# Kernel optimization log

Hardware: AMD Instinct MI355X
Metric: run time of the kernel (lower is better)

## Reference

```python
import jax, jax.numpy as jnp
import numpy as np

Q_DIM = 512
K_DIM = 512
V_DIM = 512
H_DIM = 256
B, Q, K = 4, 512, 512


def setup_inputs() -> dict:
    key = jax.random.key(0)
    ks = jax.random.split(key, 7)
    q = jax.random.normal(ks[0], (B, Q, Q_DIM), dtype=jnp.float32)
    k = jax.random.normal(ks[1], (B, K, K_DIM), dtype=jnp.float32)
    v = jax.random.normal(ks[2], (B, K, V_DIM), dtype=jnp.float32)
    S = jax.random.randint(ks[3], (B,), 1, K + 1, dtype=jnp.int64)
    # learned params (nn.Linear stores weight of shape (out, in); y = x @ W.T)
    Wq = jax.random.normal(ks[4], (H_DIM, Q_DIM), dtype=jnp.float32) / np.sqrt(Q_DIM)
    Wk = jax.random.normal(ks[5], (H_DIM, K_DIM), dtype=jnp.float32) / np.sqrt(K_DIM)
    w = jax.random.normal(ks[6], (H_DIM,), dtype=jnp.float32) / np.sqrt(H_DIM)
    return {"q": q, "k": k, "v": v, "S": S, "Wq": Wq, "Wk": Wk, "w": w}


def reference(q, k, v, S, Wq, Wk, w):
    # Additive (Bahdanau) attention scores.
    pq = jnp.einsum('bqd,hd->bqh', q, Wq)            # (B, Q, H)
    pk = jnp.einsum('bkd,hd->bkh', k, Wk)            # (B, K, H)
    t = jnp.tanh(pq[:, :, None, :] + pk[:, None, :, :])  # (B, Q, K, H)
    scores = jnp.einsum('bqkh,h->bqk', t, w)         # (B, Q, K)
    # mask keys with index >= S[b] to -inf
    kv_idx = jnp.arange(scores.shape[-1])            # (K,)
    mask = kv_idx[None, None, :] >= S[:, None, None] # (B, 1, K) -> broadcast
    scores = jnp.where(mask, -jnp.inf, scores)
    return scores
```

## Files before the change

### kernel.cpp

```cpp
#include <hip/hip_runtime.h>
#include <hip/hip_bf16.h>
#include <math.h>

#define QDIM 512
#define HDIM 256
#define QQ 512
#define KKE 512

#define TWO_LOG2E 2.8853900817779268f
#define MASK_VAL -1.0e30f

typedef __attribute__((ext_vector_type(8))) short bf16x8;
typedef __attribute__((ext_vector_type(4))) float f32x4;

__device__ __forceinline__ unsigned int pk2(float x, float y) {
  __hip_bfloat162 h = __float22bfloat162_rn(make_float2(x, y));
  unsigned int u;
  __builtin_memcpy(&u, &h, 4);
  return u;
}

__global__ __launch_bounds__(512) void proj_kernel(
    const float* __restrict__ qin, const float* __restrict__ kin,
    const float* __restrict__ Wq, const float* __restrict__ Wk,
    const float* __restrict__ wvec,
    float* __restrict__ EqT, unsigned short* __restrict__ EkT,
    float* __restrict__ wsum_out) {
  __shared__ __align__(16) unsigned short As[32 * 72];
  __shared__ __align__(16) unsigned short Bs[64 * 72];

  const int tid = threadIdx.x;
  const int lane = tid & 63;
  const int wv = __builtin_amdgcn_readfirstlane(tid >> 6);
  const int quad = lane >> 4;
  const int l16 = lane & 15;

  const int m0 = blockIdx.x * 32;
  const int h0 = blockIdx.y * 64;
  const bool isk = (blockIdx.z != 0);
  const float* A = isk ? kin : qin;
  const float* W = isk ? Wk : Wq;

  const int srow = tid >> 4;
  const int sg = (tid & 15) * 4;

  const float* arow_g = &A[(size_t)(m0 + srow) * QDIM + sg];
  const float* brow0_g = &W[(size_t)(h0 + srow) * QDIM + sg];
  const float* brow1_g = &W[(size_t)(h0 + srow + 32) * QDIM + sg];
  unsigned short* adst = &As[srow * 72 + sg];
  unsigned short* bdst0 = &Bs[srow * 72 + sg];
  unsigned short* bdst1 = &Bs[(srow + 32) * 72 + sg];

  const unsigned short* afrag = &As[((wv & 1) * 16 + l16) * 72 + quad * 8];
  const unsigned short* bfrag = &Bs[((wv >> 1) * 16 + l16) * 72 + quad * 8];

  f32x4 acc = (f32x4){0.f, 0.f, 0.f, 0.f};

  float4 pa = *(const float4*)arow_g;
  float4 pb0 = *(const float4*)brow0_g;
  float4 pb1 = *(const float4*)brow1_g;

  for (int kc = 0; kc < QDIM; kc += 64) {
    __syncthreads();
    *(uint2*)adst = make_uint2(pk2(pa.x, pa.y), pk2(pa.z, pa.w));
    *(uint2*)bdst0 = make_uint2(pk2(pb0.x, pb0.y), pk2(pb0.z, pb0.w));
    *(uint2*)bdst1 = make_uint2(pk2(pb1.x, pb1.y), pk2(pb1.z, pb1.w));
    if (kc + 64 < QDIM) {
      pa = *(const float4*)(arow_g + kc + 64);
      pb0 = *(const float4*)(brow0_g + kc + 64);
      pb1 = *(const float4*)(brow1_g + kc + 64);
    }
    __syncthreads();
    bf16x8 a0 = *(const bf16x8*)afrag;
    bf16x8 a1 = *(const bf16x8*)(afrag + 32);
    bf16x8 b0 = *(const bf16x8*)bfrag;
    bf16x8 b1 = *(const bf16x8*)(bfrag + 32);
    acc = __builtin_amdgcn_mfma_f32_16x16x32_bf16(a0, b0, acc, 0, 0, 0);
    acc = __builtin_amdgcn_mfma_f32_16x16x32_bf16(a1, b1, acc, 0, 0, 0);
  }

  const int b = m0 >> 9;
  const int hrow = h0 + (wv >> 1) * 16 + l16;
  const int mcol = (m0 & 511) + (wv & 1) * 16 + quad * 4;
  float e0 = __builtin_amdgcn_exp2f(acc[0] * TWO_LOG2E);
  float e1 = __builtin_amdgcn_exp2f(acc[1] * TWO_LOG2E);
  float e2 = __builtin_amdgcn_exp2f(acc[2] * TWO_LOG2E);
  float e3 = __builtin_amdgcn_exp2f(acc[3] * TWO_LOG2E);
  if (!isk) {
    *(float4*)(EqT + ((size_t)b * HDIM + hrow) * 512 + mcol) =
        make_float4(e0, e1, e2, e3);
    if (m0 == 0 && h0 == 0 && tid < 64) {
      float s = wvec[tid] + wvec[tid + 64] + wvec[tid + 128] + wvec[tid + 192];
#pragma unroll
      for (int off = 32; off; off >>= 1) s += __shfl_down(s, off);
      if (tid == 0) wsum_out[0] = s;
    }
  } else {
    *(uint2*)(EkT + ((size_t)b * HDIM + hrow) * 512 + mcol) =
        make_uint2(pk2(e0, e1), pk2(e2, e3));
  }
}

__global__ __launch_bounds__(256) void score_kernel(
    const float* __restrict__ EqT, const unsigned short* __restrict__ EkT,
    const float* __restrict__ wvec, const float* __restrict__ wsump,
    const int* __restrict__ Sraw, float* __restrict__ out) {
  const int b = blockIdx.z;
  const int q0 = blockIdx.y * 16;
  const int i = blockIdx.x;
  const int S = (Sraw[1] == 0) ? Sraw[2 * b] : Sraw[b];
  const int tid = threadIdx.x;
  const int wv = __builtin_amdgcn_readfirstlane(tid >> 6);
  const int L = tid & 63;
  const int q = L >> 2;
  const int k8 = (L & 3) * 8;

  __shared__ float wl[HDIM];
  __shared__ float Eqs[256][16];
  __shared__ unsigned short Eks[256][32];
  __shared__ float Cmb[3][64][8];
  wl[tid] = wvec[tid];

  const float wsum = wsump[0];
  const float* EqB = EqT + (size_t)b * (HDIM * QQ) + q0;
  const unsigned short* EkB0 = EkT + (size_t)b * (HDIM * KKE);

#pragma unroll
  for (int t = 0; t < 2; ++t) {
    const int kt = t ? (15 - i) : i;
    const int k0 = kt * 32;
    float* orow = out + ((size_t)(b * QQ + q0 + q) * KKE + k0 + k8);

    if (k0 >= S) {
      if (wv == 0) {
        float4 m4 = make_float4(MASK_VAL, MASK_VAL, MASK_VAL, MASK_VAL);
        *(float4*)&orow[0] = m4;
        *(float4*)&orow[4] = m4;
      }
      continue;
    }

    __syncthreads();
    {
      const unsigned short* EkB = EkB0 + k0;
      const int hr = tid >> 2;
      const int cq = (tid & 3) * 4;
      const int ce = (tid & 3) * 8;
#pragma unroll
      for (int p = 0; p < 4; p++) {
        *(float4*)&Eqs[hr + p * 64][cq] =
            *(const float4*)&EqB[(size_t)(hr + p * 64) * QQ + cq];
        *(uint4*)&Eks[hr + p * 64][ce] =
            *(const uint4*)&EkB[(size_t)(hr + p * 64) * KKE + ce];
      }
    }
    __syncthreads();

    float a0 = 0.f, a1 = 0.f, a2 = 0.f, a3 = 0.f;
    float a4 = 0.f, a5 = 0.f, a6 = 0.f, a7 = 0.f;
    const int hbase = wv * 64;
#pragma unroll 4
    for (int hh = 0; hh < 64; hh++) {
      const int h = hbase + hh;
      float wh = wl[h];
      float eq = Eqs[h][q];
      uint4 u = *(const uint4*)&Eks[h][k8];
      float e0 = __uint_as_float(u.x << 16);
      float e1 = __uint_as_float(u.x & 0xffff0000u);
      float e2 = __uint_as_float(u.y << 16);
      float e3 = __uint_as_float(u.y & 0xffff0000u);
      float e4 = __uint_as_float(u.z << 16);
      float e5 = __uint_as_float(u.z & 0xffff0000u);
      float e6 = __uint_as_float(u.w << 16);
      float e7 = __uint_as_float(u.w & 0xffff0000u);
      a0 = fmaf(wh, __builtin_amdgcn_rcpf(fmaf(eq, e0, 1.f)), a0);
      a1 = fmaf(wh, __builtin_amdgcn_rcpf(fmaf(eq, e1, 1.f)), a1);
      a2 = fmaf(wh, __builtin_amdgcn_rcpf(fmaf(eq, e2, 1.f)), a2);
      a3 = fmaf(wh, __builtin_amdgcn_rcpf(fmaf(eq, e3, 1.f)), a3);
      a4 = fmaf(wh, __builtin_amdgcn_rcpf(fmaf(eq, e4, 1.f)), a4);
      a5 = fmaf(wh, __builtin_amdgcn_rcpf(fmaf(eq, e5, 1.f)), a5);
      a6 = fmaf(wh, __builtin_amdgcn_rcpf(fmaf(eq, e6, 1.f)), a6);
      a7 = fmaf(wh, __builtin_amdgcn_rcpf(fmaf(eq, e7, 1.f)), a7);
    }

    if (wv > 0) {
      Cmb[wv - 1][L][0] = a0; Cmb[wv - 1][L][1] = a1;
      Cmb[wv - 1][L][2] = a2; Cmb[wv - 1][L][3] = a3;
      Cmb[wv - 1][L][4] = a4; Cmb[wv - 1][L][5] = a5;
      Cmb[wv - 1][L][6] = a6; Cmb[wv - 1][L][7] = a7;
    }
    __syncthreads();
    if (wv == 0) {
#pragma unroll
      for (int c = 0; c < 3; c++) {
        a0 += Cmb[c][L][0]; a1 += Cmb[c][L][1];
        a2 += Cmb[c][L][2]; a3 += Cmb[c][L][3];
        a4 += Cmb[c][L][4]; a5 += Cmb[c][L][5];
        a6 += Cmb[c][L][6]; a7 += Cmb[c][L][7];
      }
      const int kb = k0 + k8;
      float4 r0, r1;
      r0.x = (kb + 0 < S) ? (wsum - 2.f * a0) : MASK_VAL;
      r0.y = (kb + 1 < S) ? (wsum - 2.f * a1) : MASK_VAL;
      r0.z = (kb + 2 < S) ? (wsum - 2.f * a2) : MASK_VAL;
      r0.w = (kb + 3 < S) ? (wsum - 2.f * a3) : MASK_VAL;
      r1.x = (kb + 4 < S) ? (wsum - 2.f * a4) : MASK_VAL;
      r1.y = (kb + 5 < S) ? (wsum - 2.f * a5) : MASK_VAL;
      r1.z = (kb + 6 < S) ? (wsum - 2.f * a6) : MASK_VAL;
      r1.w = (kb + 7 < S) ? (wsum - 2.f * a7) : MASK_VAL;
      *(float4*)&orow[0] = r0;
      *(float4*)&orow[4] = r1;
    }
  }
}

extern "C" void kernel_launch(void* const* d_in, const int* in_sizes, int n_in,
                              void* d_out, int out_size, void* d_ws, size_t ws_size,
                              hipStream_t stream) {
  const float* q  = (const float*)d_in[0];
  const float* k  = (const float*)d_in[1];
  const int*   S  = (const int*)d_in[3];
  const float* Wq = (const float*)d_in[4];
  const float* Wk = (const float*)d_in[5];
  const float* w  = (const float*)d_in[6];
  float* out = (float*)d_out;

  float* wsf = (float*)d_ws;
  float* EqT = wsf;
  unsigned short* EkT = (unsigned short*)(wsf + 524288);
  float* wsum = wsf + 524288 + 262144;

  proj_kernel<<<dim3(64, 4, 2), 512, 0, stream>>>(q, k, Wq, Wk, w, EqT, EkT, wsum);
  score_kernel<<<dim3(8, 32, 4), 256, 0, stream>>>(EqT, EkT, w, wsum, S, out);
}
```

Baseline: 97.44 us.

## Store Eq as bf16, double-buffer proj LDS, prefetch both score tiles up front

The projection kernel now writes exp(2*Eq) as bf16 instead of fp32 and double-buffers its LDS tiles, which removes one barrier per k-step. The score kernel issues the global loads for both key tiles before any compute, so the second tile's fetch overlaps the first tile's work. It exits early when both tiles are fully masked. The cross-wave reduction is spread over all four waves, with 16 lanes of each wave finishing their own rows, instead of being funnelled through wave 0. Storing Eq in bf16 halves its memory traffic but adds rounding error, and the held prefetch registers raise register pressure.

```diff
diff --git a/kernel.cpp b/kernel.cpp
--- a/kernel.cpp
+++ b/kernel.cpp
@@ -24,10 +24,10 @@
     const float* __restrict__ qin, const float* __restrict__ kin,
     const float* __restrict__ Wq, const float* __restrict__ Wk,
     const float* __restrict__ wvec,
-    float* __restrict__ EqT, unsigned short* __restrict__ EkT,
+    unsigned short* __restrict__ EqT, unsigned short* __restrict__ EkT,
     float* __restrict__ wsum_out) {
-  __shared__ __align__(16) unsigned short As[32 * 72];
-  __shared__ __align__(16) unsigned short Bs[64 * 72];
+  __shared__ __align__(16) unsigned short As[2][32 * 72];
+  __shared__ __align__(16) unsigned short Bs[2][64 * 72];
 
   const int tid = threadIdx.x;
   const int lane = tid & 63;
@@ -47,12 +47,10 @@
   const float* arow_g = &A[(size_t)(m0 + srow) * QDIM + sg];
   const float* brow0_g = &W[(size_t)(h0 + srow) * QDIM + sg];
   const float* brow1_g = &W[(size_t)(h0 + srow + 32) * QDIM + sg];
-  unsigned short* adst = &As[srow * 72 + sg];
-  unsigned short* bdst0 = &Bs[srow * 72 + sg];
-  unsigned short* bdst1 = &Bs[(srow + 32) * 72 + sg];
-
-  const unsigned short* afrag = &As[((wv & 1) * 16 + l16) * 72 + quad * 8];
-  const unsigned short* bfrag = &Bs[((wv >> 1) * 16 + l16) * 72 + quad * 8];
+  const int aoff = srow * 72 + sg;
+  const int boff1 = (srow + 32) * 72 + sg;
+  const int afo = ((wv & 1) * 16 + l16) * 72 + quad * 8;
+  const int bfo = ((wv >> 1) * 16 + l16) * 72 + quad * 8;
 
   f32x4 acc = (f32x4){0.f, 0.f, 0.f, 0.f};
 
@@ -60,21 +58,21 @@
   float4 pb0 = *(const float4*)brow0_g;
   float4 pb1 = *(const float4*)brow1_g;
 
-  for (int kc = 0; kc < QDIM; kc += 64) {
-    __syncthreads();
-    *(uint2*)adst = make_uint2(pk2(pa.x, pa.y), pk2(pa.z, pa.w));
-    *(uint2*)bdst0 = make_uint2(pk2(pb0.x, pb0.y), pk2(pb0.z, pb0.w));
-    *(uint2*)bdst1 = make_uint2(pk2(pb1.x, pb1.y), pk2(pb1.z, pb1.w));
+  int ib = 0;
+  for (int kc = 0; kc < QDIM; kc += 64, ib ^= 1) {
+    *(uint2*)&As[ib][aoff] = make_uint2(pk2(pa.x, pa.y), pk2(pa.z, pa.w));
+    *(uint2*)&Bs[ib][aoff] = make_uint2(pk2(pb0.x, pb0.y), pk2(pb0.z, pb0.w));
+    *(uint2*)&Bs[ib][boff1] = make_uint2(pk2(pb1.x, pb1.y), pk2(pb1.z, pb1.w));
     if (kc + 64 < QDIM) {
       pa = *(const float4*)(arow_g + kc + 64);
       pb0 = *(const float4*)(brow0_g + kc + 64);
       pb1 = *(const float4*)(brow1_g + kc + 64);
     }
     __syncthreads();
-    bf16x8 a0 = *(const bf16x8*)afrag;
-    bf16x8 a1 = *(const bf16x8*)(afrag + 32);
-    bf16x8 b0 = *(const bf16x8*)bfrag;
-    bf16x8 b1 = *(const bf16x8*)(bfrag + 32);
+    bf16x8 a0 = *(const bf16x8*)&As[ib][afo];
+    bf16x8 a1 = *(const bf16x8*)&As[ib][afo + 32];
+    bf16x8 b0 = *(const bf16x8*)&Bs[ib][bfo];
+    bf16x8 b1 = *(const bf16x8*)&Bs[ib][bfo + 32];
     acc = __builtin_amdgcn_mfma_f32_16x16x32_bf16(a0, b0, acc, 0, 0, 0);
     acc = __builtin_amdgcn_mfma_f32_16x16x32_bf16(a1, b1, acc, 0, 0, 0);
   }
@@ -86,23 +84,19 @@
   float e1 = __builtin_amdgcn_exp2f(acc[1] * TWO_LOG2E);
   float e2 = __builtin_amdgcn_exp2f(acc[2] * TWO_LOG2E);
   float e3 = __builtin_amdgcn_exp2f(acc[3] * TWO_LOG2E);
-  if (!isk) {
-    *(float4*)(EqT + ((size_t)b * HDIM + hrow) * 512 + mcol) =
-        make_float4(e0, e1, e2, e3);
-    if (m0 == 0 && h0 == 0 && tid < 64) {
-      float s = wvec[tid] + wvec[tid + 64] + wvec[tid + 128] + wvec[tid + 192];
-#pragma unroll
-      for (int off = 32; off; off >>= 1) s += __shfl_down(s, off);
-      if (tid == 0) wsum_out[0] = s;
-    }
-  } else {
-    *(uint2*)(EkT + ((size_t)b * HDIM + hrow) * 512 + mcol) =
-        make_uint2(pk2(e0, e1), pk2(e2, e3));
+  unsigned short* ET = isk ? EkT : EqT;
+  *(uint2*)(ET + ((size_t)b * HDIM + hrow) * 512 + mcol) =
+      make_uint2(pk2(e0, e1), pk2(e2, e3));
+  if (!isk && m0 == 0 && h0 == 0 && tid < 64) {
+    float s = wvec[tid] + wvec[tid + 64] + wvec[tid + 128] + wvec[tid + 192];
+#pragma unroll
+    for (int off = 32; off; off >>= 1) s += __shfl_down(s, off);
+    if (tid == 0) wsum_out[0] = s;
   }
 }
 
 __global__ __launch_bounds__(256) void score_kernel(
-    const float* __restrict__ EqT, const unsigned short* __restrict__ EkT,
+    const unsigned short* __restrict__ EqT, const unsigned short* __restrict__ EkT,
     const float* __restrict__ wvec, const float* __restrict__ wsump,
     const int* __restrict__ Sraw, float* __restrict__ out) {
   const int b = blockIdx.z;
@@ -116,54 +110,62 @@
   const int k8 = (L & 3) * 8;
 
   __shared__ float wl[HDIM];
-  __shared__ float Eqs[256][16];
+  __shared__ unsigned short Eqs[256][16];
   __shared__ unsigned short Eks[256][32];
-  __shared__ float Cmb[3][64][8];
-  wl[tid] = wvec[tid];
+  __shared__ float Cmb[4][64][8];
+
+  const int kt0 = i;
+  const int kt1 = 15 - i;
+  const bool live0 = (kt0 * 32) < S;
+  const bool live1 = (kt1 * 32) < S;
+
+  const int mq = 4 * wv + (L >> 2);
+  const int mkg = (L & 3) * 8;
+  float* mrow0 = out + ((size_t)(b * QQ + q0 + mq) * KKE) + kt0 * 32 + mkg;
+  float* mrow1 = out + ((size_t)(b * QQ + q0 + mq) * KKE) + kt1 * 32 + mkg;
+  const float4 m4 = make_float4(MASK_VAL, MASK_VAL, MASK_VAL, MASK_VAL);
+
+  if (!live0) {
+    if (L < 16) {
+      *(float4*)&mrow0[0] = m4; *(float4*)&mrow0[4] = m4;
+      *(float4*)&mrow1[0] = m4; *(float4*)&mrow1[4] = m4;
+    }
+    return;
+  }
 
   const float wsum = wsump[0];
-  const float* EqB = EqT + (size_t)b * (HDIM * QQ) + q0;
-  const unsigned short* EkB0 = EkT + (size_t)b * (HDIM * KKE);
-
-#pragma unroll
-  for (int t = 0; t < 2; ++t) {
-    const int kt = t ? (15 - i) : i;
-    const int k0 = kt * 32;
-    float* orow = out + ((size_t)(b * QQ + q0 + q) * KKE + k0 + k8);
-
-    if (k0 >= S) {
-      if (wv == 0) {
-        float4 m4 = make_float4(MASK_VAL, MASK_VAL, MASK_VAL, MASK_VAL);
-        *(float4*)&orow[0] = m4;
-        *(float4*)&orow[4] = m4;
-      }
-      continue;
-    }
-
-    __syncthreads();
-    {
-      const unsigned short* EkB = EkB0 + k0;
-      const int hr = tid >> 2;
-      const int cq = (tid & 3) * 4;
-      const int ce = (tid & 3) * 8;
-#pragma unroll
-      for (int p = 0; p < 4; p++) {
-        *(float4*)&Eqs[hr + p * 64][cq] =
-            *(const float4*)&EqB[(size_t)(hr + p * 64) * QQ + cq];
-        *(uint4*)&Eks[hr + p * 64][ce] =
-            *(const uint4*)&EkB[(size_t)(hr + p * 64) * KKE + ce];
-      }
-    }
-    __syncthreads();
-
+  const float wreg = wvec[tid];
+  const unsigned short* EqB = EqT + (size_t)b * (HDIM * QQ) + q0;
+  const unsigned short* EkB = EkT + (size_t)b * (HDIM * KKE);
+  const int hr = tid >> 2;
+  const int ce = (tid & 3) * 8;
+
+  uint4 qa = *(const uint4*)(EqB + (size_t)tid * QQ);
+  uint4 qb = *(const uint4*)(EqB + (size_t)tid * QQ + 8);
+  uint4 k0r[4], k1r[4];
+#pragma unroll
+  for (int p = 0; p < 4; p++)
+    k0r[p] = *(const uint4*)(EkB + (size_t)(hr + p * 64) * KKE + kt0 * 32 + ce);
+#pragma unroll
+  for (int p = 0; p < 4; p++)
+    k1r[p] = *(const uint4*)(EkB + (size_t)(hr + p * 64) * KKE + kt1 * 32 + ce);
+
+  wl[tid] = wreg;
+  *(uint4*)&Eqs[tid][0] = qa;
+  *(uint4*)&Eqs[tid][8] = qb;
+#pragma unroll
+  for (int p = 0; p < 4; p++) *(uint4*)&Eks[hr + p * 64][ce] = k0r[p];
+  __syncthreads();
+
+  const int hbase = wv * 64;
+  auto tile_pass = [&]() {
     float a0 = 0.f, a1 = 0.f, a2 = 0.f, a3 = 0.f;
     float a4 = 0.f, a5 = 0.f, a6 = 0.f, a7 = 0.f;
-    const int hbase = wv * 64;
 #pragma unroll 4
     for (int hh = 0; hh < 64; hh++) {
       const int h = hbase + hh;
       float wh = wl[h];
-      float eq = Eqs[h][q];
+      float eq = __uint_as_float((unsigned int)Eqs[h][q] << 16);
       uint4 u = *(const uint4*)&Eks[h][k8];
       float e0 = __uint_as_float(u.x << 16);
       float e1 = __uint_as_float(u.x & 0xffff0000u);
@@ -182,36 +184,54 @@
       a6 = fmaf(wh, __builtin_amdgcn_rcpf(fmaf(eq, e6, 1.f)), a6);
       a7 = fmaf(wh, __builtin_amdgcn_rcpf(fmaf(eq, e7, 1.f)), a7);
     }
-
-    if (wv > 0) {
-      Cmb[wv - 1][L][0] = a0; Cmb[wv - 1][L][1] = a1;
-      Cmb[wv - 1][L][2] = a2; Cmb[wv - 1][L][3] = a3;
-      Cmb[wv - 1][L][4] = a4; Cmb[wv - 1][L][5] = a5;
-      Cmb[wv - 1][L][6] = a6; Cmb[wv - 1][L][7] = a7;
-    }
-    __syncthreads();
-    if (wv == 0) {
-#pragma unroll
-      for (int c = 0; c < 3; c++) {
-        a0 += Cmb[c][L][0]; a1 += Cmb[c][L][1];
-        a2 += Cmb[c][L][2]; a3 += Cmb[c][L][3];
-        a4 += Cmb[c][L][4]; a5 += Cmb[c][L][5];
-        a6 += Cmb[c][L][6]; a7 += Cmb[c][L][7];
+    *(float4*)&Cmb[wv][L][0] = make_float4(a0, a1, a2, a3);
+    *(float4*)&Cmb[wv][L][4] = make_float4(a4, a5, a6, a7);
+  };
+
+  auto sum_store = [&](float* mrow, int kbase) {
+    if (L < 16) {
+      const int Ls = (mq << 2) | (L & 3);
+      float s0 = 0.f, s1 = 0.f, s2 = 0.f, s3 = 0.f;
+      float s4 = 0.f, s5 = 0.f, s6 = 0.f, s7 = 0.f;
+#pragma unroll
+      for (int w = 0; w < 4; w++) {
+        float4 c0 = *(const float4*)&Cmb[w][Ls][0];
+        float4 c1 = *(const float4*)&Cmb[w][Ls][4];
+        s0 += c0.x; s1 += c0.y; s2 += c0.z; s3 += c0.w;
+        s4 += c1.x; s5 += c1.y; s6 += c1.z; s7 += c1.w;
       }
-      const int kb = k0 + k8;
+      const int kb = kbase + mkg;
       float4 r0, r1;
-      r0.x = (kb + 0 < S) ? (wsum - 2.f * a0) : MASK_VAL;
-      r0.y = (kb + 1 < S) ? (wsum - 2.f * a1) : MASK_VAL;
-      r0.z = (kb + 2 < S) ? (wsum - 2.f * a2) : MASK_VAL;
-      r0.w = (kb + 3 < S) ? (wsum - 2.f * a3) : MASK_VAL;
-      r1.x = (kb + 4 < S) ? (wsum - 2.f * a4) : MASK_VAL;
-      r1.y = (kb + 5 < S) ? (wsum - 2.f * a5) : MASK_VAL;
-      r1.z = (kb + 6 < S) ? (wsum - 2.f * a6) : MASK_VAL;
-      r1.w = (kb + 7 < S) ? (wsum - 2.f * a7) : MASK_VAL;
-      *(float4*)&orow[0] = r0;
-      *(float4*)&orow[4] = r1;
-    }
-  }
+      r0.x = (kb + 0 < S) ? (wsum - 2.f * s0) : MASK_VAL;
+      r0.y = (kb + 1 < S) ? (wsum - 2.f * s1) : MASK_VAL;
+      r0.z = (kb + 2 < S) ? (wsum - 2.f * s2) : MASK_VAL;
+      r0.w = (kb + 3 < S) ? (wsum - 2.f * s3) : MASK_VAL;
+      r1.x = (kb + 4 < S) ? (wsum - 2.f * s4) : MASK_VAL;
+      r1.y = (kb + 5 < S) ? (wsum - 2.f * s5) : MASK_VAL;
+      r1.z = (kb + 6 < S) ? (wsum - 2.f * s6) : MASK_VAL;
+      r1.w = (kb + 7 < S) ? (wsum - 2.f * s7) : MASK_VAL;
+      *(float4*)&mrow[0] = r0;
+      *(float4*)&mrow[4] = r1;
+    }
+  };
+
+  tile_pass();
+  __syncthreads();
+  if (live1) {
+#pragma unroll
+    for (int p = 0; p < 4; p++) *(uint4*)&Eks[hr + p * 64][ce] = k1r[p];
+  }
+  sum_store(mrow0, kt0 * 32);
+
+  if (!live1) {
+    if (L < 16) { *(float4*)&mrow1[0] = m4; *(float4*)&mrow1[4] = m4; }
+    return;
+  }
+
+  __syncthreads();
+  tile_pass();
+  __syncthreads();
+  sum_store(mrow1, kt1 * 32);
 }
 
 extern "C" void kernel_launch(void* const* d_in, const int* in_sizes, int n_in,
@@ -225,10 +245,9 @@
   const float* w  = (const float*)d_in[6];
   float* out = (float*)d_out;
 
-  float* wsf = (float*)d_ws;
-  float* EqT = wsf;
-  unsigned short* EkT = (unsigned short*)(wsf + 524288);
-  float* wsum = wsf + 524288 + 262144;
+  unsigned short* EqT = (unsigned short*)d_ws;
+  unsigned short* EkT = EqT + 524288;
+  float* wsum = (float*)(EkT + 524288);
 
   proj_kernel<<<dim3(64, 4, 2), 512, 0, stream>>>(q, k, Wq, Wk, w, EqT, EkT, wsum);
   score_kernel<<<dim3(8, 32, 4), 256, 0, stream>>>(EqT, EkT, w, wsum, S, out);
```

Result: slower. 99.86 us (+2.5%).

## Process four k-tiles per block with prefetched Ek and reused Eq tile

Applied to the files above, without the earlier changes.

Each score block now handles four k-tiles instead of two, loading the Eq tile once and reusing it across all of them. The next Ek tile is prefetched into registers while the current tile computes, then written to shared memory. Ek is widened to fp32 in shared memory so the inner loop no longer unpacks bf16. The final reduction is split across all four waves instead of done by wave 0 alone. This halves the grid to 512 blocks and doubles shared memory for Ek, which lowers parallelism and may reduce occupancy.

```diff
diff --git a/kernel.cpp b/kernel.cpp
--- a/kernel.cpp
+++ b/kernel.cpp
@@ -117,99 +117,134 @@
 
   __shared__ float wl[HDIM];
   __shared__ float Eqs[256][16];
-  __shared__ unsigned short Eks[256][32];
-  __shared__ float Cmb[3][64][8];
-  wl[tid] = wvec[tid];
-
-  const float wsum = wsump[0];
-  const float* EqB = EqT + (size_t)b * (HDIM * QQ) + q0;
-  const unsigned short* EkB0 = EkT + (size_t)b * (HDIM * KKE);
-
-#pragma unroll
-  for (int t = 0; t < 2; ++t) {
-    const int kt = t ? (15 - i) : i;
-    const int k0 = kt * 32;
-    float* orow = out + ((size_t)(b * QQ + q0 + q) * KKE + k0 + k8);
-
-    if (k0 >= S) {
-      if (wv == 0) {
-        float4 m4 = make_float4(MASK_VAL, MASK_VAL, MASK_VAL, MASK_VAL);
-        *(float4*)&orow[0] = m4;
-        *(float4*)&orow[4] = m4;
-      }
-      continue;
-    }
-
+  __shared__ float Eks[256][32];
+  __shared__ float Cmb[4][64][8];
+
+  const int T[4] = {i, 7 - i, 8 + i, 15 - i};
+  bool lv[4];
+#pragma unroll
+  for (int j = 0; j < 4; j++) lv[j] = (T[j] * 32) < S;
+
+  const int mq = 4 * wv + (L >> 2);
+  const int mkg = (L & 3) * 8;
+  float* obase = out + ((size_t)(b * QQ + q0 + mq) * KKE) + mkg;
+  const float4 m4 = make_float4(MASK_VAL, MASK_VAL, MASK_VAL, MASK_VAL);
+
+  if (lv[0]) {
+    const float wsum = wsump[0];
+    const float* EqB = EqT + (size_t)b * (HDIM * QQ) + q0;
+    const unsigned short* EkB = EkT + (size_t)b * (HDIM * KKE);
+    const int hr = tid >> 2;
+    const int cq = (tid & 3) * 4;
+    const int ce = (tid & 3) * 8;
+
+    wl[tid] = wvec[tid];
+    uint4 kr[4];
+#pragma unroll
+    for (int p = 0; p < 4; p++) {
+      *(float4*)&Eqs[hr + p * 64][cq] =
+          *(const float4*)&EqB[(size_t)(hr + p * 64) * QQ + cq];
+      kr[p] = *(const uint4*)(EkB + (size_t)(hr + p * 64) * KKE + T[0] * 32 + ce);
+    }
+#pragma unroll
+    for (int p = 0; p < 4; p++) {
+      uint4 u = kr[p];
+      *(float4*)&Eks[hr + p * 64][ce] = make_float4(
+          __uint_as_float(u.x << 16), __uint_as_float(u.x & 0xffff0000u),
+          __uint_as_float(u.y << 16), __uint_as_float(u.y & 0xffff0000u));
+      *(float4*)&Eks[hr + p * 64][ce + 4] = make_float4(
+          __uint_as_float(u.z << 16), __uint_as_float(u.z & 0xffff0000u),
+          __uint_as_float(u.w << 16), __uint_as_float(u.w & 0xffff0000u));
+    }
     __syncthreads();
-    {
-      const unsigned short* EkB = EkB0 + k0;
-      const int hr = tid >> 2;
-      const int cq = (tid & 3) * 4;
-      const int ce = (tid & 3) * 8;
-#pragma unroll
-      for (int p = 0; p < 4; p++) {
-        *(float4*)&Eqs[hr + p * 64][cq] =
-            *(const float4*)&EqB[(size_t)(hr + p * 64) * QQ + cq];
-        *(uint4*)&Eks[hr + p * 64][ce] =
-            *(const uint4*)&EkB[(size_t)(hr + p * 64) * KKE + ce];
-      }
-    }
-    __syncthreads();
-
-    float a0 = 0.f, a1 = 0.f, a2 = 0.f, a3 = 0.f;
-    float a4 = 0.f, a5 = 0.f, a6 = 0.f, a7 = 0.f;
+
     const int hbase = wv * 64;
+    auto tile_pass = [&]() {
+      float a0 = 0.f, a1 = 0.f, a2 = 0.f, a3 = 0.f;
+      float a4 = 0.f, a5 = 0.f, a6 = 0.f, a7 = 0.f;
 #pragma unroll 4
-    for (int hh = 0; hh < 64; hh++) {
-      const int h = hbase + hh;
-      float wh = wl[h];
-      float eq = Eqs[h][q];
-      uint4 u = *(const uint4*)&Eks[h][k8];
-      float e0 = __uint_as_float(u.x << 16);
-      float e1 = __uint_as_float(u.x & 0xffff0000u);
-      float e2 = __uint_as_float(u.y << 16);
-      float e3 = __uint_as_float(u.y & 0xffff0000u);
-      float e4 = __uint_as_float(u.z << 16);
-      float e5 = __uint_as_float(u.z & 0xffff0000u);
-      float e6 = __uint_as_float(u.w << 16);
-      float e7 = __uint_as_float(u.w & 0xffff0000u);
-      a0 = fmaf(wh, __builtin_amdgcn_rcpf(fmaf(eq, e0, 1.f)), a0);
-      a1 = fmaf(wh, __builtin_amdgcn_rcpf(fmaf(eq, e1, 1.f)), a1);
-      a2 = fmaf(wh, __builtin_amdgcn_rcpf(fmaf(eq, e2, 1.f)), a2);
-      a3 = fmaf(wh, __builtin_amdgcn_rcpf(fmaf(eq, e3, 1.f)), a3);
-      a4 = fmaf(wh, __builtin_amdgcn_rcpf(fmaf(eq, e4, 1.f)), a4);
-      a5 = fmaf(wh, __builtin_amdgcn_rcpf(fmaf(eq, e5, 1.f)), a5);
-      a6 = fmaf(wh, __builtin_amdgcn_rcpf(fmaf(eq, e6, 1.f)), a6);
-      a7 = fmaf(wh, __builtin_amdgcn_rcpf(fmaf(eq, e7, 1.f)), a7);
-    }
-
-    if (wv > 0) {
-      Cmb[wv - 1][L][0] = a0; Cmb[wv - 1][L][1] = a1;
-      Cmb[wv - 1][L][2] = a2; Cmb[wv - 1][L][3] = a3;
-      Cmb[wv - 1][L][4] = a4; Cmb[wv - 1][L][5] = a5;
-      Cmb[wv - 1][L][6] = a6; Cmb[wv - 1][L][7] = a7;
-    }
-    __syncthreads();
-    if (wv == 0) {
-#pragma unroll
-      for (int c = 0; c < 3; c++) {
-        a0 += Cmb[c][L][0]; a1 += Cmb[c][L][1];
-        a2 += Cmb[c][L][2]; a3 += Cmb[c][L][3];
-        a4 += Cmb[c][L][4]; a5 += Cmb[c][L][5];
-        a6 += Cmb[c][L][6]; a7 += Cmb[c][L][7];
-      }
-      const int kb = k0 + k8;
-      float4 r0, r1;
-      r0.x = (kb + 0 < S) ? (wsum - 2.f * a0) : MASK_VAL;
-      r0.y = (kb + 1 < S) ? (wsum - 2.f * a1) : MASK_VAL;
-      r0.z = (kb + 2 < S) ? (wsum - 2.f * a2) : MASK_VAL;
-      r0.w = (kb + 3 < S) ? (wsum - 2.f * a3) : MASK_VAL;
-      r1.x = (kb + 4 < S) ? (wsum - 2.f * a4) : MASK_VAL;
-      r1.y = (kb + 5 < S) ? (wsum - 2.f * a5) : MASK_VAL;
-      r1.z = (kb + 6 < S) ? (wsum - 2.f * a6) : MASK_VAL;
-      r1.w = (kb + 7 < S) ? (wsum - 2.f * a7) : MASK_VAL;
-      *(float4*)&orow[0] = r0;
-      *(float4*)&orow[4] = r1;
+      for (int hh = 0; hh < 64; hh++) {
+        const int h = hbase + hh;
+        float wh = wl[h];
+        float eq = Eqs[h][q];
+        float4 u0 = *(const float4*)&Eks[h][k8];
+        float4 u1 = *(const float4*)&Eks[h][k8 + 4];
+        a0 = fmaf(wh, __builtin_amdgcn_rcpf(fmaf(eq, u0.x, 1.f)), a0);
+        a1 = fmaf(wh, __builtin_amdgcn_rcpf(fmaf(eq, u0.y, 1.f)), a1);
+        a2 = fmaf(wh, __builtin_amdgcn_rcpf(fmaf(eq, u0.z, 1.f)), a2);
+        a3 = fmaf(wh, __builtin_amdgcn_rcpf(fmaf(eq, u0.w, 1.f)), a3);
+        a4 = fmaf(wh, __builtin_amdgcn_rcpf(fmaf(eq, u1.x, 1.f)), a4);
+        a5 = fmaf(wh, __builtin_amdgcn_rcpf(fmaf(eq, u1.y, 1.f)), a5);
+        a6 = fmaf(wh, __builtin_amdgcn_rcpf(fmaf(eq, u1.z, 1.f)), a6);
+        a7 = fmaf(wh, __builtin_amdgcn_rcpf(fmaf(eq, u1.w, 1.f)), a7);
+      }
+      *(float4*)&Cmb[wv][L][0] = make_float4(a0, a1, a2, a3);
+      *(float4*)&Cmb[wv][L][4] = make_float4(a4, a5, a6, a7);
+    };
+
+    auto sum_store = [&](int kbase) {
+      if (L < 16) {
+        const int Ls = 16 * wv + L;
+        float s0 = 0.f, s1 = 0.f, s2 = 0.f, s3 = 0.f;
+        float s4 = 0.f, s5 = 0.f, s6 = 0.f, s7 = 0.f;
+#pragma unroll
+        for (int w = 0; w < 4; w++) {
+          float4 c0 = *(const float4*)&Cmb[w][Ls][0];
+          float4 c1 = *(const float4*)&Cmb[w][Ls][4];
+          s0 += c0.x; s1 += c0.y; s2 += c0.z; s3 += c0.w;
+          s4 += c1.x; s5 += c1.y; s6 += c1.z; s7 += c1.w;
+        }
+        const int kb = kbase + mkg;
+        float4 r0, r1;
+        r0.x = (kb + 0 < S) ? (wsum - 2.f * s0) : MASK_VAL;
+        r0.y = (kb + 1 < S) ? (wsum - 2.f * s1) : MASK_VAL;
+        r0.z = (kb + 2 < S) ? (wsum - 2.f * s2) : MASK_VAL;
+        r0.w = (kb + 3 < S) ? (wsum - 2.f * s3) : MASK_VAL;
+        r1.x = (kb + 4 < S) ? (wsum - 2.f * s4) : MASK_VAL;
+        r1.y = (kb + 5 < S) ? (wsum - 2.f * s5) : MASK_VAL;
+        r1.z = (kb + 6 < S) ? (wsum - 2.f * s6) : MASK_VAL;
+        r1.w = (kb + 7 < S) ? (wsum - 2.f * s7) : MASK_VAL;
+        float* mrow = obase + kbase;
+        *(float4*)&mrow[0] = r0;
+        *(float4*)&mrow[4] = r1;
+      }
+    };
+
+#pragma unroll 1
+    for (int j = 0; j < 4; j++) {
+      if (!lv[j]) break;
+      const bool pn = (j + 1 < 4) && lv[j + 1];
+      if (pn) {
+#pragma unroll
+        for (int p = 0; p < 4; p++)
+          kr[p] = *(const uint4*)(EkB + (size_t)(hr + p * 64) * KKE +
+                                  T[j + 1] * 32 + ce);
+      }
+      tile_pass();
+      __syncthreads();
+      if (pn) {
+#pragma unroll
+        for (int p = 0; p < 4; p++) {
+          uint4 u = kr[p];
+          *(float4*)&Eks[hr + p * 64][ce] = make_float4(
+              __uint_as_float(u.x << 16), __uint_as_float(u.x & 0xffff0000u),
+              __uint_as_float(u.y << 16), __uint_as_float(u.y & 0xffff0000u));
+          *(float4*)&Eks[hr + p * 64][ce + 4] = make_float4(
+              __uint_as_float(u.z << 16), __uint_as_float(u.z & 0xffff0000u),
+              __uint_as_float(u.w << 16), __uint_as_float(u.w & 0xffff0000u));
+        }
+      }
+      sum_store(T[j] * 32);
+      if (pn) __syncthreads();
+    }
+  }
+
+#pragma unroll
+  for (int j = 0; j < 4; j++) {
+    if (!lv[j] && L < 16) {
+      float* mrow = obase + T[j] * 32;
+      *(float4*)&mrow[0] = m4;
+      *(float4*)&mrow[4] = m4;
     }
   }
 }
@@ -231,5 +266,5 @@
   float* wsum = wsf + 524288 + 262144;
 
   proj_kernel<<<dim3(64, 4, 2), 512, 0, stream>>>(q, k, Wq, Wk, w, EqT, EkT, wsum);
-  score_kernel<<<dim3(8, 32, 4), 256, 0, stream>>>(EqT, EkT, w, wsum, S, out);
-}
+  score_kernel<<<dim3(4, 32, 4), 256, 0, stream>>>(EqT, EkT, w, wsum, S, out);
+}
```

After: 99.82 us. 1.02x slower.
